# Kernel tuning notes

Measured on AMD Instinct MI355X. Metric: run time of the kernel, lower is better.

Reference implementation:

```python
import jax, jax.numpy as jnp
import numpy as np

N_NTYPES, N_ETYPES, H, D = 3, 5, 8, 32
N, E, C = 50000, 300000, 256


def setup_inputs() -> dict:
    key = jax.random.key(0)
    ks = jax.random.split(key, 13)
    s_c = 1.0 / np.sqrt(C)
    s_d = 1.0 / np.sqrt(D)
    return {
        "x": jax.random.normal(ks[0], (N, C), jnp.float32),
        "Wk": jax.random.normal(ks[1], (N_NTYPES, C, C), jnp.float32) * s_c,
        "Wq": jax.random.normal(ks[2], (N_NTYPES, C, C), jnp.float32) * s_c,
        "Wv": jax.random.normal(ks[3], (N_NTYPES, C, C), jnp.float32) * s_c,
        "Ratt": jax.random.normal(ks[4], (N_ETYPES, H, D, D), jnp.float32) * s_d,
        "Rmsg": jax.random.normal(ks[5], (N_ETYPES, H, D, D), jnp.float32) * s_d,
        "pri": jax.random.uniform(ks[6], (N_ETYPES, H), jnp.float32),
        "Wa": jax.random.normal(ks[7], (N_NTYPES, C, C), jnp.float32) * s_c,
        "skip": jax.random.normal(ks[8], (N_NTYPES,), jnp.float32),
        "src": jax.random.randint(ks[9], (E,), 0, N),
        "dst": jax.random.randint(ks[10], (E,), 0, N),
        "etype": jax.random.randint(ks[11], (E,), 0, N_ETYPES),
        "ntype": jax.random.randint(ks[12], (N,), 0, N_NTYPES),
    }


def typed_linear(x, W, types, n_types):
    # per-row weight selection by type; loop over small fixed #types
    out = jnp.zeros((x.shape[0], W.shape[-1]), x.dtype)
    for t in range(n_types):
        out = out + jnp.where((types == t)[:, None], x @ W[t], 0.0)
    return out


def reference(x, Wk, Wq, Wv, Ratt, Rmsg, pri, Wa, skip, src, dst, etype, ntype):
    n = x.shape[0]
    k = typed_linear(x, Wk, ntype, N_NTYPES).reshape(n, H, D)
    q = typed_linear(x, Wq, ntype, N_NTYPES).reshape(n, H, D)
    v = typed_linear(x, Wv, ntype, N_NTYPES).reshape(n, H, D)

    k_e = k[src]   # [E,H,D]
    v_e = v[src]   # [E,H,D]
    q_e = q[dst]   # [E,H,D]

    # per-edge-type, per-head DxD relation transforms (loop over small fixed #etypes)
    kw = jnp.zeros_like(k_e)
    mv = jnp.zeros_like(v_e)
    for r in range(N_ETYPES):
        m = (etype == r)[:, None, None]
        kw = kw + jnp.where(m, jnp.einsum('ehd,hdf->ehf', k_e, Ratt[r]), 0.0)
        mv = mv + jnp.where(m, jnp.einsum('ehd,hdf->ehf', v_e, Rmsg[r]), 0.0)

    # attention logits [E,H]
    a = (kw * q_e).sum(-1) * pri[etype] / jnp.sqrt(jnp.asarray(D, x.dtype))

    # edge softmax over incoming edges of each dst node, per head
    amax = jax.ops.segment_max(a, dst, num_segments=n)
    ex = jnp.exp(a - amax[dst])
    denom = jax.ops.segment_sum(ex, dst, num_segments=n)
    attn = ex / denom[dst]

    # weighted scatter-sum aggregation
    h = jax.ops.segment_sum(mv * attn[..., None], dst, num_segments=n)
    h = h.reshape(n, H * D)

    # typed output projection + sigmoid-gated skip (in_size == H*D)
    h = typed_linear(h, Wa, ntype, N_NTYPES)
    alpha = jax.nn.sigmoid(skip)[ntype][:, None]
    return h * alpha + x * (1.0 - alpha)
```

## Files before the change

kernel.cpp:

```cpp
#include <hip/hip_runtime.h>
#include <math.h>

#define CDIM 256
#define HD 8
#define DD 32
#define NT 3
#define ET 5
#define QWC (ET * CDIM)

typedef unsigned short u16;
typedef __attribute__((ext_vector_type(8))) short s16x8;
typedef __attribute__((ext_vector_type(4))) float f32x4;

__device__ __forceinline__ float b2f(u16 u) { return __uint_as_float(((unsigned)u) << 16); }
__device__ __forceinline__ u16 f2b(float x) {
    unsigned u = __float_as_uint(x);
    return (u16)((u + 0x7FFF + ((u >> 16) & 1)) >> 16);
}

__global__ void bhist_k(const int* __restrict__ ntype, int N, int nblk, int* __restrict__ bcnt) {
    __shared__ int wc[4][NT];
    int b = blockIdx.x, tid = threadIdx.x, lane = tid & 63, w = tid >> 6;
    int i = b * 256 + tid;
    int t = (i < N) ? ntype[i] : -1;
#pragma unroll
    for (int r = 0; r < NT; ++r) {
        unsigned long long m = __ballot(t == r);
        if (lane == 0) wc[w][r] = __popcll(m);
    }
    __syncthreads();
    if (tid < NT) bcnt[tid * nblk + b] = wc[0][tid] + wc[1][tid] + wc[2][tid] + wc[3][tid];
}

__global__ void bscan_k(const int* __restrict__ bcnt, int* __restrict__ base,
                        int* __restrict__ off, int total, int nblk, int N) {
    __shared__ int s[1024];
    int t = threadIdx.x;
    int v = (t < total) ? bcnt[t] : 0;
    s[t] = v; __syncthreads();
    for (int o = 1; o < 1024; o <<= 1) {
        int u = (t >= o) ? s[t - o] : 0; __syncthreads();
        s[t] += u; __syncthreads();
    }
    if (t < total) base[t] = s[t] - v;
    if (t < NT) off[t] = s[t * nblk] - bcnt[t * nblk];
    if (t == NT) off[NT] = N;
}

__global__ void bscatter_k(const int* __restrict__ ntype, int N, int nblk,
                           const int* __restrict__ base, int* __restrict__ perm) {
    __shared__ int wc[4][NT];
    __shared__ int woff[4][NT];
    int b = blockIdx.x, tid = threadIdx.x, lane = tid & 63, w = tid >> 6;
    int i = b * 256 + tid;
    int t = (i < N) ? ntype[i] : -1;
    unsigned long long mlt = (1ULL << lane) - 1;
    int rank = 0;
#pragma unroll
    for (int r = 0; r < NT; ++r) {
        unsigned long long m = __ballot(t == r);
        if (lane == 0) wc[w][r] = __popcll(m);
        if (t == r) rank = __popcll(m & mlt);
    }
    __syncthreads();
    if (tid == 0) {
#pragma unroll
        for (int r = 0; r < NT; ++r) {
            int a = 0;
#pragma unroll
            for (int w0 = 0; w0 < 4; ++w0) { woff[w0][r] = a; a += wc[w0][r]; }
        }
    }
    __syncthreads();
    if (t >= 0) perm[base[t * nblk + b] + woff[w][t] + rank] = i;
}

__global__ void ehist_k(const int* __restrict__ dst, const int* __restrict__ etype, int E,
                        int* __restrict__ khist) {
    int i = blockIdx.x * 256 + threadIdx.x;
    if (i < E) atomicAdd(&khist[dst[i] * ET + etype[i]], 1);
}

__global__ void kscan1_k(const int* __restrict__ khist, int* __restrict__ kscan,
                         int* __restrict__ bsum, int KEYS) {
    __shared__ int s[256];
    int b = blockIdx.x, t = threadIdx.x, i = b * 256 + t;
    int v = (i < KEYS) ? khist[i] : 0;
    s[t] = v; __syncthreads();
    for (int o = 1; o < 256; o <<= 1) {
        int u = (t >= o) ? s[t - o] : 0; __syncthreads();
        s[t] += u; __syncthreads();
    }
    if (i < KEYS) kscan[i] = s[t] - v;
    if (t == 255) bsum[b] = s[t];
}

__global__ void kscan2_k(int* __restrict__ bsum, int NB) {
    __shared__ int s[1024];
    int t = threadIdx.x;
    int v = (t < NB) ? bsum[t] : 0;
    s[t] = v; __syncthreads();
    for (int o = 1; o < 1024; o <<= 1) {
        int u = (t >= o) ? s[t - o] : 0; __syncthreads();
        s[t] += u; __syncthreads();
    }
    if (t < NB) bsum[t] = s[t] - v;
}

__global__ void kscan3r_k(int* __restrict__ kscan, const int* __restrict__ bsum,
                          int* __restrict__ rowptr, int KEYS, int E) {
    int i = blockIdx.x * 256 + threadIdx.x;
    if (i < KEYS) {
        int v = kscan[i] + bsum[blockIdx.x];
        kscan[i] = v;
        rowptr[i] = v;
    }
    if (i == 0) rowptr[KEYS] = E;
}

__global__ void escatter_k(const int* __restrict__ src, const int* __restrict__ dst,
                           const int* __restrict__ etype, int E,
                           int* __restrict__ kscan, int* __restrict__ epay) {
    int e = blockIdx.x * 256 + threadIdx.x;
    if (e < E) {
        int et = etype[e];
        int pos = atomicAdd(&kscan[dst[e] * ET + et], 1);
        epay[pos] = (et << 24) | src[e];
    }
}

__global__ void f2bv_k(const float* __restrict__ in, u16* __restrict__ out, size_t n4) {
    size_t i = (size_t)blockIdx.x * 256 + threadIdx.x;
    if (i >= n4) return;
    float4 v = ((const float4*)in)[i];
    ushort4 o; o.x = f2b(v.x); o.y = f2b(v.y); o.z = f2b(v.z); o.w = f2b(v.w);
    ((ushort4*)out)[i] = o;
}

__global__ __launch_bounds__(256) void wconv2_k(const float* __restrict__ Wk,
                                                const float* __restrict__ Wv,
                                                u16* __restrict__ Wtb) {
    __shared__ u16 s[64][72];
    int k0 = blockIdx.x * 64, c0 = blockIdx.y * 64, z = blockIdx.z;
    const float* Wp = (z < NT) ? (Wk + (size_t)z * CDIM * CDIM)
                               : (Wv + (size_t)(z - NT) * CDIM * CDIM);
    int r = threadIdx.x >> 2, q = (threadIdx.x & 3) * 16;
#pragma unroll
    for (int m = 0; m < 16; m += 4) {
        float4 v = *(const float4*)(Wp + (size_t)(k0 + r) * CDIM + c0 + q + m);
        s[r][q + m + 0] = f2b(v.x); s[r][q + m + 1] = f2b(v.y);
        s[r][q + m + 2] = f2b(v.z); s[r][q + m + 3] = f2b(v.w);
    }
    __syncthreads();
    int c = threadIdx.x >> 2, kq = (threadIdx.x & 3) * 16;
    u16* op = Wtb + ((size_t)z * CDIM + c0 + c) * CDIM + k0 + kq;
#pragma unroll
    for (int m = 0; m < 16; m += 4) {
        ushort4 o;
        o.x = s[kq + m + 0][c]; o.y = s[kq + m + 1][c];
        o.z = s[kq + m + 2][c]; o.w = s[kq + m + 3][c];
        *(ushort4*)(op + m) = o;
    }
}

__global__ __launch_bounds__(256) void rfold_k(const float* __restrict__ Wq,
                                               const float* __restrict__ Ratt,
                                               u16* __restrict__ qf_b,
                                               const float* __restrict__ Wa,
                                               const float* __restrict__ Rmsg,
                                               u16* __restrict__ af_b) {
    __shared__ float Rs[DD][DD];
    int b = blockIdx.x;
    int t = b / (ET * HD);
    int eh = b % (ET * HD);
    int et = eh >> 3, h = eh & 7;
    int tid = threadIdx.x;

    if (blockIdx.y == 0) {
        float4 rv = ((const float4*)(Ratt + (size_t)eh * (DD * DD)))[tid];
        int r = tid >> 3, c4 = (tid & 7) * 4;
        Rs[r][c4 + 0] = rv.x; Rs[r][c4 + 1] = rv.y;
        Rs[r][c4 + 2] = rv.z; Rs[r][c4 + 3] = rv.w;
        __syncthreads();

        int c = tid;
        const float* wr = Wq + (size_t)t * (CDIM * CDIM) + (size_t)c * CDIM + h * DD;
        float wrow[DD];
#pragma unroll
        for (int f = 0; f < DD; f += 4) {
            float4 v = *(const float4*)(wr + f);
            wrow[f] = v.x; wrow[f + 1] = v.y; wrow[f + 2] = v.z; wrow[f + 3] = v.w;
        }
        for (int m = 0; m < DD; ++m) {
            float acc = 0.f;
#pragma unroll
            for (int f = 0; f < DD; ++f) acc += wrow[f] * Rs[m][f];
            qf_b[((size_t)t * QWC + et * 256 + h * 32 + m) * CDIM + c] = f2b(acc);
        }
    } else {
        float4 rv = ((const float4*)(Rmsg + (size_t)eh * (DD * DD)))[tid];
        int r = tid >> 3, c4 = (tid & 7) * 4;
        Rs[r][c4 + 0] = rv.x; Rs[r][c4 + 1] = rv.y;
        Rs[r][c4 + 2] = rv.z; Rs[r][c4 + 3] = rv.w;
        __syncthreads();

        int col = tid;
        float wcol[DD];
#pragma unroll
        for (int m = 0; m < DD; ++m)
            wcol[m] = Wa[(size_t)t * (CDIM * CDIM) + (size_t)(h * 32 + m) * CDIM + col];

        u16* op = af_b + ((size_t)t * CDIM + col) * QWC + et * 256 + h * 32;
        for (int f = 0; f < DD; ++f) {
            float acc = 0.f;
#pragma unroll
            for (int m = 0; m < DD; ++m) acc += Rs[f][m] * wcol[m];
            op[f] = f2b(acc);
        }
    }
}

__global__ __launch_bounds__(256) void gemmall_k(
    const u16* __restrict__ xb, const u16* __restrict__ wtb, const u16* __restrict__ qf_b,
    u16* __restrict__ kb, u16* __restrict__ vb, u16* __restrict__ qwsv,
    const int* __restrict__ perm, const int* __restrict__ off, int N, int bpt, int npanel)
{
    __shared__ u16 As[64][40];
    __shared__ u16 Bs[128][40];
    __shared__ int ridx[64];

    int bid = blockIdx.x;
    int xcd = bid & 7;
    int rr_ = bid >> 3;
    int g = rr_ / 14, bx = rr_ % 14;
    int p = g * 8 + xcd;
    if (p >= npanel) return;
    int t = p / bpt, bi = p % bpt;

    int i0 = off[t] + bi * 64, iend = off[t + 1];
    if (i0 >= iend) return;
    int tid = threadIdx.x;

    u16* out; int ostr, oc0; const u16* bslab;
    const size_t CC = (size_t)CDIM * CDIM;
    if (bx < 2)      { out = kb;   ostr = CDIM; oc0 = bx * 128;       bslab = wtb + (size_t)t * CC; }
    else if (bx < 4) { out = vb;   ostr = CDIM; oc0 = (bx - 2) * 128; bslab = wtb + (size_t)(NT + t) * CC; }
    else             { out = qwsv; ostr = QWC;  oc0 = (bx - 4) * 128; bslab = qf_b + (size_t)t * QWC * CDIM; }

    if (tid < 64) ridx[tid] = (i0 + tid < iend) ? perm[i0 + tid] : -1;
    __syncthreads();

    int sr = tid >> 2, sq = (tid & 3) * 8;
    int srB = tid >> 1, sqB = (tid & 1) * 16;
    int ar = ridx[sr];
    const u16* asrc = xb + (size_t)(ar < 0 ? 0 : ar) * CDIM + sq;
    const u16* bsrc = bslab + (size_t)(oc0 + srB) * CDIM + sqB;

    int lane = tid & 63, wid = tid >> 6;
    int wr = wid >> 1, wc = wid & 1;
    int l15 = lane & 15, lk = (lane >> 4) * 8;

    f32x4 acc[2][4];
#pragma unroll
    for (int mi = 0; mi < 2; ++mi)
#pragma unroll
        for (int j = 0; j < 4; ++j)
            acc[mi][j] = (f32x4){0.f, 0.f, 0.f, 0.f};

    uint4 apre = make_uint4(0, 0, 0, 0);
    if (ar >= 0) apre = *(const uint4*)(asrc);
    uint4 bp0 = *(const uint4*)(bsrc);
    uint4 bp1 = *(const uint4*)(bsrc + 8);

    for (int k0 = 0; k0 < CDIM; k0 += 32) {
        __syncthreads();
        *(uint4*)&As[sr][sq] = apre;
        *(uint4*)&Bs[srB][sqB] = bp0;
        *(uint4*)&Bs[srB][sqB + 8] = bp1;
        __syncthreads();

        if (k0 + 32 < CDIM) {
            if (ar >= 0) apre = *(const uint4*)(asrc + k0 + 32);
            bp0 = *(const uint4*)(bsrc + k0 + 32);
            bp1 = *(const uint4*)(bsrc + k0 + 40);
        }

        s16x8 af0 = *(const s16x8*)&As[wr * 32 + l15][lk];
        s16x8 af1 = *(const s16x8*)&As[wr * 32 + 16 + l15][lk];
#pragma unroll
        for (int j = 0; j < 4; ++j) {
            s16x8 bf = *(const s16x8*)&Bs[wc * 64 + j * 16 + l15][lk];
            acc[0][j] = __builtin_amdgcn_mfma_f32_16x16x32_bf16(af0, bf, acc[0][j], 0, 0, 0);
            acc[1][j] = __builtin_amdgcn_mfma_f32_16x16x32_bf16(af1, bf, acc[1][j], 0, 0, 0);
        }
    }

    int rbase = wr * 32 + (lane >> 4) * 4;
#pragma unroll
    for (int mi = 0; mi < 2; ++mi) {
#pragma unroll
        for (int r = 0; r < 4; ++r) {
            int node = ridx[rbase + mi * 16 + r];
            if (node < 0) continue;
            size_t b0 = (size_t)node * ostr + oc0 + wc * 64 + l15;
#pragma unroll
            for (int j = 0; j < 4; ++j)
                out[b0 + j * 16] = f2b(acc[mi][j][r]);
        }
    }
}

__global__ __launch_bounds__(256) void outgemm_k(
    const u16* __restrict__ svn, const u16* __restrict__ af_b, float* __restrict__ out,
    const int* __restrict__ perm, const int* __restrict__ off, int N, int bpt,
    const float* __restrict__ x, const float* __restrict__ skip)
{
    __shared__ u16 As[64][68];
    __shared__ int ridx[64];

    int t = blockIdx.x / bpt, bi = blockIdx.x % bpt;
    int i0 = off[t] + bi * 64, iend = off[t + 1];
    if (i0 >= iend) return;
    int tid = threadIdx.x;
    if (tid < 64) ridx[tid] = (i0 + tid < iend) ? perm[i0 + tid] : -1;
    __syncthreads();

    int lane = tid & 63, y = tid >> 6;
    int l15 = lane & 15, lq = lane >> 4;
    int lk = lq * 8;

    int sr = tid >> 2, sc = (tid & 3) * 16;
    int ar = ridx[sr];
    const u16* asrc = svn + (size_t)(ar < 0 ? 0 : ar) * QWC + sc;
    const u16* bbase = af_b + ((size_t)t * CDIM + y * 64) * QWC;

    f32x4 acc[4][4];
#pragma unroll
    for (int mi = 0; mi < 4; ++mi)
#pragma unroll
        for (int ci = 0; ci < 4; ++ci)
            acc[mi][ci] = (f32x4){0.f, 0.f, 0.f, 0.f};

    uint4 apre0 = make_uint4(0, 0, 0, 0), apre1 = make_uint4(0, 0, 0, 0);
    if (ar >= 0) {
        apre0 = *(const uint4*)(asrc);
        apre1 = *(const uint4*)(asrc + 8);
    }

    for (int kc = 0; kc < 20; ++kc) {
        __syncthreads();
        *(uint4*)&As[sr][sc] = apre0;
        *(uint4*)&As[sr][sc + 8] = apre1;
        __syncthreads();
        if (kc + 1 < 20) {
            int ko = (kc + 1) * 64;
            if (ar >= 0) {
                apre0 = *(const uint4*)(asrc + ko);
                apre1 = *(const uint4*)(asrc + ko + 8);
            }
        }

        int kbase = kc * 64;
        s16x8 bf0[4], bf1[4];
#pragma unroll
        for (int ci = 0; ci < 4; ++ci) {
            const u16* bp = bbase + (size_t)(ci * 16 + l15) * QWC + kbase;
            bf0[ci] = *(const s16x8*)(bp + lk);
            bf1[ci] = *(const s16x8*)(bp + 32 + lk);
        }

#pragma unroll
        for (int mi = 0; mi < 4; ++mi) {
            s16x8 af0 = *(const s16x8*)&As[mi * 16 + l15][lk];
            s16x8 af1 = *(const s16x8*)&As[mi * 16 + l15][32 + lk];
#pragma unroll
            for (int ci = 0; ci < 4; ++ci) {
                acc[mi][ci] = __builtin_amdgcn_mfma_f32_16x16x32_bf16(af0, bf0[ci], acc[mi][ci], 0, 0, 0);
                acc[mi][ci] = __builtin_amdgcn_mfma_f32_16x16x32_bf16(af1, bf1[ci], acc[mi][ci], 0, 0, 0);
            }
        }
    }

    float alpha = 1.f / (1.f + __expf(-skip[t]));
    float beta = 1.f - alpha;
#pragma unroll
    for (int mi = 0; mi < 4; ++mi) {
#pragma unroll
        for (int r = 0; r < 4; ++r) {
            int node = ridx[mi * 16 + lq * 4 + r];
            if (node < 0) continue;
#pragma unroll
            for (int ci = 0; ci < 4; ++ci) {
                size_t b0 = (size_t)node * CDIM + y * 64 + ci * 16 + l15;
                out[b0] = acc[mi][ci][r] * alpha + x[b0] * beta;
            }
        }
    }
}

__global__ __launch_bounds__(256) void gather3_k(
    const u16* __restrict__ kb, const u16* __restrict__ vb, u16* __restrict__ qwsv,
    const float* __restrict__ pri, const int* __restrict__ rowptr, const int* __restrict__ epay,
    int N)
{
    int d = (blockIdx.x * 256 + threadIdx.x) >> 6;
    if (d >= N) return;
    int lane = threadIdx.x & 63, h = lane >> 3;
    const float rsD = 0.17677669529663687f;
    size_t rowb = (size_t)d * QWC + lane * 4;

    ushort4 qu0 = *(const ushort4*)(qwsv + rowb);
    ushort4 qu1 = *(const ushort4*)(qwsv + rowb + 256);
    ushort4 qu2 = *(const ushort4*)(qwsv + rowb + 512);
    ushort4 qu3 = *(const ushort4*)(qwsv + rowb + 768);
    ushort4 qu4 = *(const ushort4*)(qwsv + rowb + 1024);

    int p0 = __builtin_amdgcn_readfirstlane(rowptr[d * ET]);
    int p1 = __builtin_amdgcn_readfirstlane(rowptr[d * ET + ET]);

    float Sv0[4] = {0,0,0,0}, Sv1[4] = {0,0,0,0}, Sv2[4] = {0,0,0,0};
    float Sv3[4] = {0,0,0,0}, Sv4[4] = {0,0,0,0};
    float a0 = 0.f, a1 = 0.f, a2 = 0.f, a3 = 0.f, dsum = 0.f;
    int cur_et = -1;
    float cq0 = 0.f, cq1 = 0.f, cq2 = 0.f, cq3 = 0.f, cpf = 0.f;

    int payc = 0; ushort4 kuc = {0,0,0,0}, vuc = {0,0,0,0};
    if (p0 < p1) {
        payc = epay[p0];
        int s = payc & 0xFFFFFF;
        kuc = *(const ushort4*)(kb + (size_t)s * CDIM + lane * 4);
        vuc = *(const ushort4*)(vb + (size_t)s * CDIM + lane * 4);
    }

    for (int p = p0; p < p1; ++p) {
        int payn = 0; ushort4 kun = {0,0,0,0}, vun = {0,0,0,0};
        if (p + 1 < p1) {
            payn = epay[p + 1];
            int sn = payn & 0xFFFFFF;
            kun = *(const ushort4*)(kb + (size_t)sn * CDIM + lane * 4);
            vun = *(const ushort4*)(vb + (size_t)sn * CDIM + lane * 4);
        }
        int et = __builtin_amdgcn_readfirstlane(payc) >> 24;
        if (et != cur_et) {
            switch (cur_et) {
                case 0: Sv0[0]=a0; Sv0[1]=a1; Sv0[2]=a2; Sv0[3]=a3; break;
                case 1: Sv1[0]=a0; Sv1[1]=a1; Sv1[2]=a2; Sv1[3]=a3; break;
                case 2: Sv2[0]=a0; Sv2[1]=a1; Sv2[2]=a2; Sv2[3]=a3; break;
                case 3: Sv3[0]=a0; Sv3[1]=a1; Sv3[2]=a2; Sv3[3]=a3; break;
                default: break;
            }
            a0 = a1 = a2 = a3 = 0.f;
            cur_et = et;
            ushort4 q = (et == 0) ? qu0 : (et == 1) ? qu1 : (et == 2) ? qu2
                       : (et == 3) ? qu3 : qu4;
            cq0 = b2f(q.x); cq1 = b2f(q.y); cq2 = b2f(q.z); cq3 = b2f(q.w);
            cpf = pri[et * HD + h] * rsD;
        }
        float t = b2f(kuc.x) * cq0 + b2f(kuc.y) * cq1 + b2f(kuc.z) * cq2 + b2f(kuc.w) * cq3;
        t += __shfl_xor(t, 1, 8);
        t += __shfl_xor(t, 2, 8);
        t += __shfl_xor(t, 4, 8);
        float ex = __expf(t * cpf);
        a0 += ex * b2f(vuc.x); a1 += ex * b2f(vuc.y);
        a2 += ex * b2f(vuc.z); a3 += ex * b2f(vuc.w);
        dsum += ex;
        payc = payn; kuc = kun; vuc = vun;
    }
    switch (cur_et) {
        case 0: Sv0[0]=a0; Sv0[1]=a1; Sv0[2]=a2; Sv0[3]=a3; break;
        case 1: Sv1[0]=a0; Sv1[1]=a1; Sv1[2]=a2; Sv1[3]=a3; break;
        case 2: Sv2[0]=a0; Sv2[1]=a1; Sv2[2]=a2; Sv2[3]=a3; break;
        case 3: Sv3[0]=a0; Sv3[1]=a1; Sv3[2]=a2; Sv3[3]=a3; break;
        case 4: Sv4[0]=a0; Sv4[1]=a1; Sv4[2]=a2; Sv4[3]=a3; break;
        default: break;
    }

    float inv = dsum > 0.f ? 1.f / dsum : 0.f;
    ushort4 o;
    o.x=f2b(Sv0[0]*inv); o.y=f2b(Sv0[1]*inv); o.z=f2b(Sv0[2]*inv); o.w=f2b(Sv0[3]*inv);
    *(ushort4*)(qwsv + rowb) = o;
    o.x=f2b(Sv1[0]*inv); o.y=f2b(Sv1[1]*inv); o.z=f2b(Sv1[2]*inv); o.w=f2b(Sv1[3]*inv);
    *(ushort4*)(qwsv + rowb + 256) = o;
    o.x=f2b(Sv2[0]*inv); o.y=f2b(Sv2[1]*inv); o.z=f2b(Sv2[2]*inv); o.w=f2b(Sv2[3]*inv);
    *(ushort4*)(qwsv + rowb + 512) = o;
    o.x=f2b(Sv3[0]*inv); o.y=f2b(Sv3[1]*inv); o.z=f2b(Sv3[2]*inv); o.w=f2b(Sv3[3]*inv);
    *(ushort4*)(qwsv + rowb + 768) = o;
    o.x=f2b(Sv4[0]*inv); o.y=f2b(Sv4[1]*inv); o.z=f2b(Sv4[2]*inv); o.w=f2b(Sv4[3]*inv);
    *(ushort4*)(qwsv + rowb + 1024) = o;
}

extern "C" void kernel_launch(void* const* d_in, const int* in_sizes, int n_in,
                              void* d_out, int out_size, void* d_ws, size_t ws_size,
                              hipStream_t stream) {
    const float* x    = (const float*)d_in[0];
    const float* Wk   = (const float*)d_in[1];
    const float* Wq   = (const float*)d_in[2];
    const float* Wv   = (const float*)d_in[3];
    const float* Ratt = (const float*)d_in[4];
    const float* Rmsg = (const float*)d_in[5];
    const float* pri  = (const float*)d_in[6];
    const float* Wa   = (const float*)d_in[7];
    const float* skip = (const float*)d_in[8];
    const int* src   = (const int*)d_in[9];
    const int* dst   = (const int*)d_in[10];
    const int* etype = (const int*)d_in[11];
    const int* ntype = (const int*)d_in[12];

    int N = in_sizes[12];
    int E = in_sizes[9];
    const size_t NC = (size_t)N * CDIM;
    const int KEYS = N * ET;
    const int NB = (KEYS + 255) / 256;
    const int nblk = (N + 255) / 256;
    const size_t WTE = (size_t)NT * CDIM * CDIM;
    const size_t QFE = (size_t)NT * QWC * CDIM;

    u16* kb   = (u16*)d_ws;
    u16* vb   = kb + NC;
    u16* qwsv = vb + NC;
    u16* wtb  = qwsv + 5 * NC;
    u16* qf_b = wtb + 2 * WTE;
    u16* af_b = qf_b + QFE;
    int* rowptr = (int*)(af_b + QFE);
    int* perm   = rowptr + KEYS + 1;
    int* epay   = perm + N;
    int* off    = epay + E;
    int* khist = (int*)qwsv;
    int* kscan = khist + KEYS;
    int* bsum  = kscan + KEYS;
    int* bcnt  = bsum + 1024;
    int* base  = bcnt + NT * nblk;

    u16* xb = (u16*)d_out;

    hipMemsetAsync(khist, 0, (size_t)KEYS * sizeof(int), stream);

    bhist_k<<<nblk, 256, 0, stream>>>(ntype, N, nblk, bcnt);
    bscan_k<<<1, 1024, 0, stream>>>(bcnt, base, off, NT * nblk, nblk, N);
    bscatter_k<<<nblk, 256, 0, stream>>>(ntype, N, nblk, base, perm);

    ehist_k<<<(E + 255) / 256, 256, 0, stream>>>(dst, etype, E, khist);
    kscan1_k<<<NB, 256, 0, stream>>>(khist, kscan, bsum, KEYS);
    kscan2_k<<<1, 1024, 0, stream>>>(bsum, NB);
    kscan3r_k<<<NB, 256, 0, stream>>>(kscan, bsum, rowptr, KEYS, E);
    escatter_k<<<(E + 255) / 256, 256, 0, stream>>>(src, dst, etype, E, kscan, epay);

    wconv2_k<<<dim3(4, 4, 2 * NT), 256, 0, stream>>>(Wk, Wv, wtb);
    rfold_k<<<dim3(NT * ET * HD, 2), 256, 0, stream>>>(Wq, Ratt, qf_b, Wa, Rmsg, af_b);
    size_t n4 = NC / 4;
    f2bv_k<<<(int)((n4 + 255) / 256), 256, 0, stream>>>(x, xb, n4);

    int bpt = (N + 63) / 64;
    int npanel = NT * bpt;
    int ppad = (npanel + 7) & ~7;

    gemmall_k<<<ppad * 14, 256, 0, stream>>>(xb, wtb, qf_b, kb, vb, qwsv,
                                             perm, off, N, bpt, npanel);

    gather3_k<<<(N * 64 + 255) / 256, 256, 0, stream>>>(kb, vb, qwsv, pri, rowptr, epay, N);

    outgemm_k<<<NT * bpt, 256, 0, stream>>>(qwsv, af_b, (float*)d_out, perm, off, N, bpt,
                                            x, skip);
}
```

Baseline: 397.6 us.

## Split output GEMM into column quarters with XCD-aware panel mapping

The output projection kernel is split so each block computes a 64-row by 64-column tile instead of 64x256. This launches four times as many blocks, and block IDs are remapped so that the four column blocks of a panel share an XCD, which should improve L2 reuse of the A panel. Each wave now holds one B fragment pair that is prefetched one step ahead, so register pressure drops and occupancy should rise. In exchange, each A row tile is reloaded from global memory four times, and there is more per-block overhead.

After: 385.9 us. 1.03x faster.

```diff
diff --git a/kernel.cpp b/kernel.cpp
--- a/kernel.cpp
+++ b/kernel.cpp
@@ -312,13 +312,19 @@
 
 __global__ __launch_bounds__(256) void outgemm_k(
     const u16* __restrict__ svn, const u16* __restrict__ af_b, float* __restrict__ out,
-    const int* __restrict__ perm, const int* __restrict__ off, int N, int bpt,
+    const int* __restrict__ perm, const int* __restrict__ off, int N, int bpt, int npanel,
     const float* __restrict__ x, const float* __restrict__ skip)
 {
     __shared__ u16 As[64][68];
     __shared__ int ridx[64];
 
-    int t = blockIdx.x / bpt, bi = blockIdx.x % bpt;
+    int bid = blockIdx.x;
+    int xcd = bid & 7;
+    int rr_ = bid >> 3;
+    int g = rr_ / 4, cx = rr_ % 4;
+    int p = g * 8 + xcd;
+    if (p >= npanel) return;
+    int t = p / bpt, bi = p % bpt;
     int i0 = off[t] + bi * 64, iend = off[t + 1];
     if (i0 >= iend) return;
     int tid = threadIdx.x;
@@ -328,56 +334,48 @@
     int lane = tid & 63, y = tid >> 6;
     int l15 = lane & 15, lq = lane >> 4;
     int lk = lq * 8;
+    int colb = cx * 64 + y * 16;
 
     int sr = tid >> 2, sc = (tid & 3) * 16;
     int ar = ridx[sr];
     const u16* asrc = svn + (size_t)(ar < 0 ? 0 : ar) * QWC + sc;
-    const u16* bbase = af_b + ((size_t)t * CDIM + y * 64) * QWC;
-
-    f32x4 acc[4][4];
-#pragma unroll
-    for (int mi = 0; mi < 4; ++mi)
-#pragma unroll
-        for (int ci = 0; ci < 4; ++ci)
-            acc[mi][ci] = (f32x4){0.f, 0.f, 0.f, 0.f};
+    const u16* brow = af_b + ((size_t)t * CDIM + colb + l15) * QWC;
+
+    f32x4 acc[4];
+#pragma unroll
+    for (int mi = 0; mi < 4; ++mi) acc[mi] = (f32x4){0.f, 0.f, 0.f, 0.f};
 
     uint4 apre0 = make_uint4(0, 0, 0, 0), apre1 = make_uint4(0, 0, 0, 0);
     if (ar >= 0) {
         apre0 = *(const uint4*)(asrc);
         apre1 = *(const uint4*)(asrc + 8);
     }
+    s16x8 bf0 = *(const s16x8*)(brow + lk);
+    s16x8 bf1 = *(const s16x8*)(brow + 32 + lk);
 
     for (int kc = 0; kc < 20; ++kc) {
         __syncthreads();
         *(uint4*)&As[sr][sc] = apre0;
         *(uint4*)&As[sr][sc + 8] = apre1;
         __syncthreads();
+
+        s16x8 b0c = bf0, b1c = bf1;
         if (kc + 1 < 20) {
             int ko = (kc + 1) * 64;
             if (ar >= 0) {
                 apre0 = *(const uint4*)(asrc + ko);
                 apre1 = *(const uint4*)(asrc + ko + 8);
             }
-        }
-
-        int kbase = kc * 64;
-        s16x8 bf0[4], bf1[4];
-#pragma unroll
-        for (int ci = 0; ci < 4; ++ci) {
-            const u16* bp = bbase + (size_t)(ci * 16 + l15) * QWC + kbase;
-            bf0[ci] = *(const s16x8*)(bp + lk);
-            bf1[ci] = *(const s16x8*)(bp + 32 + lk);
+            bf0 = *(const s16x8*)(brow + ko + lk);
+            bf1 = *(const s16x8*)(brow + ko + 32 + lk);
         }
 
 #pragma unroll
         for (int mi = 0; mi < 4; ++mi) {
             s16x8 af0 = *(const s16x8*)&As[mi * 16 + l15][lk];
             s16x8 af1 = *(const s16x8*)&As[mi * 16 + l15][32 + lk];
-#pragma unroll
-            for (int ci = 0; ci < 4; ++ci) {
-                acc[mi][ci] = __builtin_amdgcn_mfma_f32_16x16x32_bf16(af0, bf0[ci], acc[mi][ci], 0, 0, 0);
-                acc[mi][ci] = __builtin_amdgcn_mfma_f32_16x16x32_bf16(af1, bf1[ci], acc[mi][ci], 0, 0, 0);
-            }
+            acc[mi] = __builtin_amdgcn_mfma_f32_16x16x32_bf16(af0, b0c, acc[mi], 0, 0, 0);
+            acc[mi] = __builtin_amdgcn_mfma_f32_16x16x32_bf16(af1, b1c, acc[mi], 0, 0, 0);
         }
     }
 
@@ -389,11 +387,8 @@
         for (int r = 0; r < 4; ++r) {
             int node = ridx[mi * 16 + lq * 4 + r];
             if (node < 0) continue;
-#pragma unroll
-            for (int ci = 0; ci < 4; ++ci) {
-                size_t b0 = (size_t)node * CDIM + y * 64 + ci * 16 + l15;
-                out[b0] = acc[mi][ci][r] * alpha + x[b0] * beta;
-            }
+            size_t b0 = (size_t)node * CDIM + colb + l15;
+            out[b0] = acc[mi][r] * alpha + x[b0] * beta;
         }
     }
 }
@@ -559,6 +554,6 @@
 
     gather3_k<<<(N * 64 + 255) / 256, 256, 0, stream>>>(kb, vb, qwsv, pri, rowptr, epay, N);
 
-    outgemm_k<<<NT * bpt, 256, 0, stream>>>(qwsv, af_b, (float*)d_out, perm, off, N, bpt,
-                                            x, skip);
-}
+    outgemm_k<<<ppad * 4, 256, 0, stream>>>(qwsv, af_b, (float*)d_out, perm, off, N, bpt,
+                                            npanel, x, skip);
+}
```
